# Optimization experiments

Measured on AMD Instinct MI355X. Metric: run time of the kernel, lower is better.

Reference implementation:

```python
import jax, jax.numpy as jnp
import numpy as np

V, E, H = 50000, 256, 256   # vocab, emb_dim, hid_dim
R, S, W = 64, 32, 64        # reviews, sentences/review, words/sentence
UF = 20                     # user feature dim


def _bigru_last(x, wih, whh, bih, bhh):
    """Bidirectional GRU over x [B,T,D]; returns sum of final hidden states of
    the two directions, shape [B,H]. Params stacked over direction axis 0."""
    Hh = whh.shape[-1]

    def onedir(xd, wi, wh, bi, bh):
        gx = jnp.einsum('btd,gd->btg', xd, wi) + bi  # [B,T,3H] input gates precomputed

        def step(h, gxt):
            gh = h @ wh.T + bh
            r = jax.nn.sigmoid(gxt[:, :Hh] + gh[:, :Hh])
            z = jax.nn.sigmoid(gxt[:, Hh:2 * Hh] + gh[:, Hh:2 * Hh])
            n = jnp.tanh(gxt[:, 2 * Hh:] + r * gh[:, 2 * Hh:])
            return (1.0 - z) * n + z * h, None

        h0 = jnp.zeros((xd.shape[0], Hh), xd.dtype)
        hT, _ = jax.lax.scan(step, h0, jnp.swapaxes(gx, 0, 1))
        return hT

    return (onedir(x, wih[0], whh[0], bih[0], bhh[0])
            + onedir(x[:, ::-1], wih[1], whh[1], bih[1], bhh[1]))


def setup_inputs() -> dict:
    key = jax.random.key(0)
    ks = iter(jax.random.split(key, 40))

    def wmat(shape, scale=0.05):
        return jax.random.normal(next(ks), shape, jnp.float32) * scale

    inp = {}
    inp['inputs'] = jax.random.randint(next(ks), (R, S, W), 0, V)
    inp['sent_lengths'] = jax.random.randint(next(ks), (R, S), 1, W)
    inp['sent_counts'] = jax.random.randint(next(ks), (R,), 1, S)
    inp['user_feats'] = jax.random.normal(next(ks), (R, UF), jnp.float32)
    inp['embed'] = wmat((V, E))
    for name, din in (('wg', E), ('sg', H), ('rg', H + UF)):
        inp[name + '_wih'] = wmat((2, 3 * H, din))
        inp[name + '_whh'] = wmat((2, 3 * H, H))
        inp[name + '_bih'] = jnp.zeros((2, 3 * H), jnp.float32)
        inp[name + '_bhh'] = jnp.zeros((2, 3 * H), jnp.float32)
    inp['rfc_w1'] = wmat((H // 2, H + UF)); inp['rfc_b1'] = jnp.zeros((H // 2,), jnp.float32)
    inp['rfc_w2'] = wmat((1, H // 2));      inp['rfc_b2'] = jnp.zeros((1,), jnp.float32)
    inp['pfc_w1'] = wmat((H // 2, H));      inp['pfc_b1'] = jnp.zeros((H // 2,), jnp.float32)
    inp['pfc_w2'] = wmat((9, H // 2));      inp['pfc_b2'] = jnp.zeros((9,), jnp.float32)
    inp['uf_w'] = jnp.ones((UF,), jnp.float32)  # user_feats_weights
    return inp


def reference(inputs, sent_lengths, sent_counts, user_feats, embed,
              wg_wih, wg_whh, wg_bih, wg_bhh,
              sg_wih, sg_whh, sg_bih, sg_bhh,
              rg_wih, rg_whh, rg_bih, rg_bhh,
              rfc_w1, rfc_b1, rfc_w2, rfc_b2,
              pfc_w1, pfc_b1, pfc_w2, pfc_b2, uf_w):
    Rr, Sr, Wr = inputs.shape
    emb = embed[inputs]  # [R,S,W,E]  (dropout = identity in eval mode)
    # word-level bi-GRU, all R*S sentences batched together
    sent = _bigru_last(emb.reshape(Rr * Sr, Wr, emb.shape[-1]),
                       wg_wih, wg_whh, wg_bih, wg_bhh).reshape(Rr, Sr, -1)
    # sentence-level bi-GRU, batch over reviews
    rev = _bigru_last(sent, sg_wih, sg_whh, sg_bih, sg_bhh)  # [R,H]
    # F.normalize(user_feats) * user_feats_weights
    nrm = jnp.maximum(jnp.linalg.norm(user_feats, axis=-1, keepdims=True), 1e-12)
    p_batch = jnp.concatenate([rev, (user_feats / nrm) * uf_w], axis=-1)  # [R,H+20]
    r_stars = (jax.nn.selu(p_batch @ rfc_w1.T + rfc_b1) @ rfc_w2.T + rfc_b2)[:, 0]  # [R]
    # review-level bi-GRU over the sequence of reviews (batch 1)
    doc = _bigru_last(p_batch[None], rg_wih, rg_whh, rg_bih, rg_bhh)[0]  # [H]
    p_stars = jax.nn.selu(doc @ pfc_w1.T + pfc_b1) @ pfc_w2.T + pfc_b2  # [9]
    return p_stars, r_stars
```

## Files before the change

kernel.cpp:

```cpp
#include <hip/hip_runtime.h>
#include <math.h>

#define R_ 64
#define S_ 32
#define W_ 64
#define H_ 256
#define UF_ 20
#define TC 4

typedef short bf16x8 __attribute__((ext_vector_type(8)));
typedef float f32x4  __attribute__((ext_vector_type(4)));

#define MFMA(a,b,c) __builtin_amdgcn_mfma_f32_16x16x32_bf16((a),(b),(c),0,0,0)

typedef const unsigned int __attribute__((address_space(1)))* gp_t;
typedef unsigned int __attribute__((address_space(3)))* lp_t;
#define GLOAD16(SRC, DST) \
  __builtin_amdgcn_global_load_lds((gp_t)(const void*)(SRC), (lp_t)(void*)(DST), 16, 0, 0)

#define SW(r) ((((r)>>1)&7)<<3)

#define BFRAG(ff) ((ff) < 40 ? Breg[(ff) < 40 ? (ff) : 0] \
                 : *(const bf16x8*)&Bl[w][(ff) >= 40 ? (ff)-40 : 0][l*8])

__device__ __forceinline__ float sigf(float x){ return 1.0f/(1.0f+__expf(-x)); }
__device__ __forceinline__ float tanhf_(float x){ float e=__expf(2.0f*x); return 1.0f-2.0f/(e+1.0f); }
__device__ __forceinline__ float seluf_(float x){
  const float sc=1.0507009873554805f, al=1.6732632423543772f;
  return x>0.0f ? sc*x : sc*al*(expf(x)-1.0f);
}
__device__ __forceinline__ short tobf(float f){
  unsigned u=__float_as_uint(f); u += 0x7fffu + ((u>>16)&1u); return (short)(u>>16);
}
__device__ __forceinline__ float bf2f(short s){
  return __uint_as_float(((unsigned)(unsigned short)s) << 16);
}
__device__ __forceinline__ unsigned pk2(float a, float b){
  return (unsigned)(unsigned short)tobf(a) | ((unsigned)(unsigned short)tobf(b) << 16);
}

__global__ void prep_word_w(const float* __restrict__ wih, const float* __restrict__ whh,
                            short* __restrict__ Bw)
{
  int idx = blockIdx.x*256 + threadIdx.x;
  int lane = idx & 63;
  int rest = idx >> 6;
  int f  = rest % 6;  rest /= 6;
  int kt = rest % 16; rest /= 16;
  int w  = rest % 8;
  int d  = rest / 8;
  int gate = f >> 1;
  int j = 32*w + (f&1)*16 + (lane&15);
  int row = gate*256 + j;
  const float* W = (kt < 8 ? wih : whh) + (size_t)d*768*256;
  int k = (kt&7)*32 + (lane>>4)*8;
  short* dst = Bw + ((((size_t)(d*8 + w)*16 + kt)*6 + f)*64 + lane)*8;
#pragma unroll
  for (int jj=0;jj<8;jj++) dst[jj] = tobf(W[(size_t)row*256 + k + jj]);
}

__global__ void prep_rnn_w(const float* __restrict__ whh, short* __restrict__ Bs)
{
  int idx = blockIdx.x*256 + threadIdx.x;
  int lane = idx & 63;
  int rest = idx >> 6;
  int f  = rest % 6; rest /= 6;
  int kt = rest % 8; rest /= 8;
  int w  = rest % 8;
  int d  = rest / 8;
  int j = 32*w + (f&1)*16 + (lane&15);
  int row = (f>>1)*256 + j;
  const float* W = whh + (size_t)d*768*256;
  int k = kt*32 + (lane>>4)*8;
  short* dst = Bs + ((((size_t)(d*8 + w)*8 + kt)*6 + f)*64 + lane)*8;
#pragma unroll
  for (int jj=0;jj<8;jj++) dst[jj] = tobf(W[(size_t)row*256 + k + jj]);
}

__global__ void prep_gemm_w(const float* __restrict__ Wsrc, short* __restrict__ Bg)
{
  int idx = blockIdx.x*256 + threadIdx.x;
  int lane = idx & 63;
  int rest = idx >> 6;
  int kt = rest % 8;
  int nt = rest / 8;
  int n = nt*16 + (lane&15);
  int k = kt*32 + (lane>>4)*8;
  short* dst = Bg + (((size_t)nt*8 + kt)*64 + lane)*8;
#pragma unroll
  for (int jj=0;jj<8;jj++) dst[jj] = tobf(Wsrc[(size_t)n*256 + k + jj]);
}

__global__ __launch_bounds__(256) void gemm_gxu(
    const short* __restrict__ Ab, const float* __restrict__ Af,
    const int* __restrict__ toks, const short* __restrict__ Bg,
    const float* __restrict__ bih, const float* __restrict__ bhh,
    short* __restrict__ C, long Czoff,
    int mode, int t0, int Mclamp, int Cstride)
{
  const int z  = blockIdx.z;
  const int m0 = blockIdx.x * 64;
  const int yt = blockIdx.y * 8;
  const int ntb = (mode == 2 ? z*48 : 0) + yt;
  const int tid = threadIdx.x;
  const int w = tid >> 6, l = tid & 63;
  const int c = l & 15, q = l >> 4;
  __shared__ short As[64][264];
  {
    const int row = tid >> 2, c0 = (tid & 3) * 64;
    if (mode == 0) {
      const uint4* s = (const uint4*)(Ab + (size_t)(m0+row)*256 + c0);
#pragma unroll
      for (int i = 0; i < 8; i++) *(uint4*)&As[row][c0 + i*8] = s[i];
    } else {
      int r;
      if (mode == 1) {
        r = m0 + row; if (r >= Mclamp) r = Mclamp - 1;
      } else {
        const int rr = m0 + row;
        const int s_ = rr / TC, i_ = rr % TC;
        const int wd = z ? (63 - (t0 + i_)) : (t0 + i_);
        r = toks[s_*64 + wd];
      }
      const float* s = Af + (size_t)r*256 + c0;
#pragma unroll
      for (int i = 0; i < 8; i++) {
        float4 v0 = *(const float4*)(s + i*8);
        float4 v1 = *(const float4*)(s + i*8 + 4);
        uint4 u;
        u.x = pk2(v0.x, v0.y); u.y = pk2(v0.z, v0.w);
        u.z = pk2(v1.x, v1.y); u.w = pk2(v1.z, v1.w);
        *(uint4*)&As[row][c0 + i*8] = u;
      }
    }
  }
  float bias[2];
#pragma unroll
  for (int nt = 0; nt < 2; nt++) {
    const int coln = (yt + 2*w + nt)*16 + c;
    const int bidx = (mode == 2 ? z*768 : 0) + coln;
    bias[nt] = bih[bidx] + ((bidx % 768) < 512 ? bhh[bidx] : 0.0f);
  }
  __syncthreads();
  f32x4 acc[4][2];
#pragma unroll
  for (int a = 0; a < 4; a++) { acc[a][0] = (f32x4)0.f; acc[a][1] = (f32x4)0.f; }
#pragma unroll
  for (int kt = 0; kt < 8; kt++) {
    const int ko = kt*32 + q*8;
    bf16x8 a0 = *(const bf16x8*)&As[ 0+c][ko];
    bf16x8 a1 = *(const bf16x8*)&As[16+c][ko];
    bf16x8 a2 = *(const bf16x8*)&As[32+c][ko];
    bf16x8 a3 = *(const bf16x8*)&As[48+c][ko];
    bf16x8 b0 = *(const bf16x8*)&Bg[(((size_t)(ntb + 2*w    )*8 + kt)*64 + l)*8];
    bf16x8 b1 = *(const bf16x8*)&Bg[(((size_t)(ntb + 2*w + 1)*8 + kt)*64 + l)*8];
    acc[0][0]=MFMA(a0,b0,acc[0][0]); acc[1][0]=MFMA(a1,b0,acc[1][0]);
    acc[2][0]=MFMA(a2,b0,acc[2][0]); acc[3][0]=MFMA(a3,b0,acc[3][0]);
    acc[0][1]=MFMA(a0,b1,acc[0][1]); acc[1][1]=MFMA(a1,b1,acc[1][1]);
    acc[2][1]=MFMA(a2,b1,acc[2][1]); acc[3][1]=MFMA(a3,b1,acc[3][1]);
  }
  short* Cz = C + (size_t)z * Czoff;
#pragma unroll
  for (int mt = 0; mt < 4; mt++)
#pragma unroll
  for (int nt = 0; nt < 2; nt++)
#pragma unroll
  for (int rg = 0; rg < 4; rg++)
    Cz[(size_t)(m0 + mt*16 + q*4 + rg)*Cstride + (yt + 2*w + nt)*16 + c] =
        tobf(acc[mt][nt][rg] + bias[nt]);
}

__device__ __forceinline__ void stage_issue(
    short* dstbase,
    int mode, int d, int g, int w, int l,
    int nwords, int t0, int tt,
    const int* tokp, const short* gxF, const short* gxB)
{
  const char* bF = (const char*)gxF;
  const char* bB = (const char*)gxB;
#pragma unroll
  for (int i = 0; i < 3; i++) {
    const int off = i*1024 + l*16;
    const int rl  = (off >= 1536) ? 1 : 0;
    const int col = off - rl*1536;
    const char* src;
    if (mode == 0) {
      const int tx  = d ? (nwords - 1 - tt) : tt;
      const int tok = tokp[(2*w + rl)*64 + tx];
      src = bF + (size_t)tok*3072 + d*1536 + col;
    } else if (mode == 1) {
      const int ri = (g*16 + 2*w + rl)*TC + (tt - t0);
      src = (d ? bB : bF) + (size_t)ri*1536 + col;
    } else {
      const int se  = d ? (nwords - 1 - tt) : tt;
      const int row = g*16 + 2*w + rl;
      src = bF + ((size_t)row*nwords + se)*3072 + (size_t)d*1536 + col;
    }
    GLOAD16(src, dstbase + (size_t)w*1536 + i*512);
  }
}

__global__ __launch_bounds__(512, 2) void gru_rec(
    const int* __restrict__ toks,
    const short* __restrict__ gxF, const short* __restrict__ gxB,
    const short* __restrict__ Bh, int wstride, int koff,
    const float* __restrict__ bhh,
    float* __restrict__ hstate, int NS,
    int t0, int nsteps, int mode, int nwords)
{
  const int d = blockIdx.x & 1;
  const int g = blockIdx.x >> 1;
  const int tid = threadIdx.x;
  const int w = tid >> 6, l = tid & 63;
  const int c = l & 15, q = l >> 4;

  __shared__ short gbuf[2][16][768];
  __shared__ short hbf[2][16][264];
  __shared__ short Bl[8][8][512];
  __shared__ int   tokL[1024];

  if (mode == 0)
    for (int i = tid; i < 1024; i += 512) tokL[i] = toks[(size_t)g*1024 + i];

  bf16x8 Breg[40];
  {
    const short* Bb = Bh + (size_t)(d*8 + w)*wstride + (size_t)koff*3072 + l*8;
#pragma unroll
    for (int ff = 0; ff < 48; ff++) {
      bf16x8 v = *(const bf16x8*)(Bb + ff*512);
      if (ff < 40) Breg[ff] = v;
      else *(bf16x8*)&Bl[w][ff-40][l*8] = v;
    }
  }

  float bNH[2];
#pragma unroll
  for (int jt = 0; jt < 2; jt++)
    bNH[jt] = bhh[d*768 + 512 + 32*w + jt*16 + c];

  float hst[2][4];
  const int cur0 = t0 & 1;
  if (t0 == 0) {
#pragma unroll
    for (int a = 0; a < 2; a++)
#pragma unroll
    for (int r = 0; r < 4; r++) hst[a][r] = 0.0f;
  } else {
#pragma unroll
    for (int jt = 0; jt < 2; jt++)
#pragma unroll
    for (int rg = 0; rg < 4; rg++)
      hst[jt][rg] = hstate[((size_t)d*NS + g*16 + q*4 + rg)*256 + 32*w + jt*16 + c];
  }
#pragma unroll
  for (int jt = 0; jt < 2; jt++)
#pragma unroll
  for (int rg = 0; rg < 4; rg++)
    hbf[cur0][q*4 + rg][32*w + jt*16 + c] = tobf(hst[jt][rg]);

  stage_issue((short*)gbuf[cur0], mode, d, g, w, l, nwords, t0, t0,
              (mode == 0) ? toks + (size_t)g*1024 : (const int*)nullptr, gxF, gxB);

  __syncthreads();

  const int tend = t0 + nsteps;
  for (int t = t0; t < tend; t++) {
    const int cur = t & 1, nxt = 1 - cur;

    if (t + 1 < tend)
      stage_issue((short*)gbuf[nxt], mode, d, g, w, l, nwords, t0, t + 1,
                  tokL, gxF, gxB);

    f32x4 accR[2], accZ[2], accNH[2];
#pragma unroll
    for (int a = 0; a < 2; a++) { accR[a]=(f32x4)0.f; accZ[a]=(f32x4)0.f; accNH[a]=(f32x4)0.f; }
#pragma unroll
    for (int kt = 0; kt < 8; kt++) {
      bf16x8 a0 = *(const bf16x8*)&hbf[cur][c][kt*32 + q*8];
      bf16x8 b0 = BFRAG(kt*6+0), b1 = BFRAG(kt*6+1), b2 = BFRAG(kt*6+2),
             b3 = BFRAG(kt*6+3), b4 = BFRAG(kt*6+4), b5 = BFRAG(kt*6+5);
      accR[0]=MFMA(a0,b0,accR[0]);  accR[1]=MFMA(a0,b1,accR[1]);
      accZ[0]=MFMA(a0,b2,accZ[0]);  accZ[1]=MFMA(a0,b3,accZ[1]);
      accNH[0]=MFMA(a0,b4,accNH[0]); accNH[1]=MFMA(a0,b5,accNH[1]);
    }

#pragma unroll
    for (int jt = 0; jt < 2; jt++)
#pragma unroll
    for (int rg = 0; rg < 4; rg++) {
      const int m = q*4 + rg;
      const int j = 32*w + jt*16 + c;
      const float gr = bf2f(gbuf[cur][m][j]);
      const float gz = bf2f(gbuf[cur][m][256 + j]);
      const float gn = bf2f(gbuf[cur][m][512 + j]);
      const float r = sigf(gr + accR[jt][rg]);
      const float z = sigf(gz + accZ[jt][rg]);
      const float n = tanhf_(gn + r*(accNH[jt][rg] + bNH[jt]));
      float h = hst[jt][rg];
      h = (1.0f - z)*n + z*h;
      hst[jt][rg] = h;
      hbf[nxt][m][j] = tobf(h);
    }
    __syncthreads();
  }

#pragma unroll
  for (int jt = 0; jt < 2; jt++)
#pragma unroll
  for (int rg = 0; rg < 4; rg++)
    hstate[((size_t)d*NS + g*16 + q*4 + rg)*256 + 32*w + jt*16 + c] = hst[jt][rg];
}

__global__ void add2bf(const float* __restrict__ a, const float* __restrict__ b,
                       short* __restrict__ o)
{
  int i = (blockIdx.x*256 + threadIdx.x)*4;
  float4 x = *(const float4*)&a[i];
  float4 y = *(const float4*)&b[i];
  *(uint2*)&o[i] = make_uint2(pk2(x.x+y.x, x.y+y.y), pk2(x.z+y.z, x.w+y.w));
}

__global__ __launch_bounds__(512, 2) void rev_gru(
    const float* __restrict__ gx, const short* __restrict__ Br,
    const float* __restrict__ bhh,
    float* __restrict__ doc)
{
  const int d = blockIdx.x;
  const int tid = threadIdx.x;
  const int w = tid >> 6, l = tid & 63;
  const int c = l & 15, q = l >> 4;
  const int j0 = 32*w + c;

  __shared__ short hbf[2][16][256];
  __shared__ short Bl[8][8][512];
  for (int i = tid; i < 2*16*256; i += 512) ((short*)hbf)[i] = 0;

  bf16x8 Breg[40];
  {
    const short* Bbase = Br + (size_t)(d*8 + w)*8*6*512 + l*8;
#pragma unroll
    for (int ff = 0; ff < 48; ff++) {
      bf16x8 v = *(const bf16x8*)(Bbase + ff*512);
      if (ff < 40) Breg[ff] = v;
      else *(bf16x8*)&Bl[w][ff-40][l*8] = v;
    }
  }

  float bNH[2];
#pragma unroll
  for (int jt = 0; jt < 2; jt++)
    bNH[jt] = bhh[d*768 + 512 + j0 + jt*16];

  float hst[2];
  hst[0] = 0.0f; hst[1] = 0.0f;
  __syncthreads();

  for (int t = 0; t < 64; t++) {
    const int cur = t & 1, nxt = 1 - cur;
    const int teff = (d == 0) ? t : (63 - t);

    float G[2][3];
    if (q == 0) {
#pragma unroll
      for (int jt = 0; jt < 2; jt++) {
        const size_t row = (size_t)teff*1536 + d*768;
        const int j = j0 + jt*16;
        G[jt][0] = gx[row + j]; G[jt][1] = gx[row + 256 + j]; G[jt][2] = gx[row + 512 + j];
      }
    }

    f32x4 accR[2], accZ[2], accNH[2];
#pragma unroll
    for (int a=0;a<2;a++) { accR[a]=(f32x4)0.f; accZ[a]=(f32x4)0.f; accNH[a]=(f32x4)0.f; }
#pragma unroll
    for (int kt = 0; kt < 8; kt++) {
      bf16x8 a0 = *(const bf16x8*)&hbf[cur][c][(kt*32 + q*8) ^ SW(c)];
      bf16x8 b0 = BFRAG(kt*6+0), b1 = BFRAG(kt*6+1), b2 = BFRAG(kt*6+2),
             b3 = BFRAG(kt*6+3), b4 = BFRAG(kt*6+4), b5 = BFRAG(kt*6+5);
      accR[0]=MFMA(a0,b0,accR[0]);  accR[1]=MFMA(a0,b1,accR[1]);
      accZ[0]=MFMA(a0,b2,accZ[0]);  accZ[1]=MFMA(a0,b3,accZ[1]);
      accNH[0]=MFMA(a0,b4,accNH[0]); accNH[1]=MFMA(a0,b5,accNH[1]);
    }

    if (q == 0) {
#pragma unroll
      for (int jt = 0; jt < 2; jt++) {
        const float r = sigf(G[jt][0] + accR[jt][0]);
        const float z = sigf(G[jt][1] + accZ[jt][0]);
        const float n = tanhf_(G[jt][2] + r*(accNH[jt][0] + bNH[jt]));
        const float h = n + z*(hst[jt] - n);
        hst[jt] = h;
        hbf[nxt][0][j0 + jt*16] = tobf(h);
      }
    }
    __syncthreads();
  }
  if (q == 0) {
#pragma unroll
    for (int jt = 0; jt < 2; jt++)
      doc[d*256 + j0 + jt*16] = hst[jt];
  }
}

__global__ __launch_bounds__(256) void gemm_nt16(
    const float* __restrict__ A, const float* __restrict__ B,
    const float* __restrict__ bih, const float* __restrict__ bhh,
    float* __restrict__ C, int M, int N, int K)
{
  const int m0 = blockIdx.x * 16;
  const int n0 = blockIdx.y * 64;
  const int tid = threadIdx.x;
  __shared__ float As[16][17];
  __shared__ float Bs[16][68];
  float acc[4] = {0,0,0,0};
  const int m  = tid >> 4, n4 = (tid & 15) * 4;
  const int bn = tid >> 2, bk = (tid & 3) * 4;
  for (int k0 = 0; k0 < K; k0 += 16) {
    const int ak = tid & 15;
    float av = (k0 + ak < K) ? A[(size_t)(m0+m)*K + k0 + ak] : 0.0f;
    float4 b4 = make_float4(0,0,0,0);
    if (k0 + bk < K) b4 = *(const float4*)&B[(size_t)(n0+bn)*K + k0 + bk];
    __syncthreads();
    As[ak][m] = av;
    Bs[bk+0][bn]=b4.x; Bs[bk+1][bn]=b4.y; Bs[bk+2][bn]=b4.z; Bs[bk+3][bn]=b4.w;
    __syncthreads();
#pragma unroll
    for (int k = 0; k < 16; k++) {
      const float a = As[k][m];
      const float4 bb = *(const float4*)&Bs[k][n4];
      acc[0]+=a*bb.x; acc[1]+=a*bb.y; acc[2]+=a*bb.z; acc[3]+=a*bb.w;
    }
  }
#pragma unroll
  for (int i = 0; i < 4; i++) {
    const int n = n0 + n4 + i;
    acc[i] += bih[n] + ((n % 768) < 512 ? bhh[n] : 0.0f);
  }
  *(float4*)&C[(size_t)(m0+m)*N + n0+n4] = make_float4(acc[0],acc[1],acc[2],acc[3]);
}

__global__ void pbatch_k(const float* __restrict__ hs, const float* __restrict__ uf,
                         const float* __restrict__ ufw, float* __restrict__ pb)
{
  const int r = blockIdx.x, tid = threadIdx.x;
  __shared__ float nrm;
  if (tid == 0) {
    float s = 0.f;
    for (int i = 0; i < UF_; i++) { const float v = uf[r*UF_ + i]; s += v*v; }
    nrm = fmaxf(sqrtf(s), 1e-12f);
  }
  __syncthreads();
  if (tid < H_)  pb[r*276 + tid] = hs[r*H_ + tid] + hs[(size_t)R_*H_ + r*H_ + tid];
  if (tid < UF_) pb[r*276 + H_ + tid] = uf[r*UF_ + tid] / nrm * ufw[tid];
}

__global__ void rstars_k(const float* __restrict__ pb,
                         const float* __restrict__ w1, const float* __restrict__ b1,
                         const float* __restrict__ w2, const float* __restrict__ b2,
                         float* __restrict__ out)
{
  const int r = blockIdx.x, tid = threadIdx.x;
  __shared__ float ps[276];
  __shared__ float s1[128];
  for (int i = tid; i < 276; i += 128) ps[i] = pb[r*276 + i];
  __syncthreads();
  float a = b1[tid];
  for (int k = 0; k < 276; k++) a += ps[k] * w1[tid*276 + k];
  s1[tid] = seluf_(a);
  __syncthreads();
  if (tid == 0) {
    float s = b2[0];
    for (int k = 0; k < 128; k++) s += s1[k] * w2[k];
    out[9 + r] = s;
  }
}

__global__ void pstars_k(const float* __restrict__ doc2,
                         const float* __restrict__ w1, const float* __restrict__ b1,
                         const float* __restrict__ w2, const float* __restrict__ b2,
                         float* __restrict__ out)
{
  const int tid = threadIdx.x;
  __shared__ float dc[256];
  __shared__ float s1[128];
  dc[tid]       = doc2[tid];
  dc[128 + tid] = doc2[128 + tid];
  __syncthreads();
  float a = b1[tid];
  for (int k = 0; k < 256; k++) a += dc[k] * w1[tid*256 + k];
  s1[tid] = seluf_(a);
  __syncthreads();
  if (tid < 9) {
    float s = b2[tid];
    for (int k = 0; k < 128; k++) s += s1[k] * w2[tid*128 + k];
    out[tid] = s;
  }
}

__global__ void docsum_k(float* __restrict__ doc)
{
  const int tid = threadIdx.x;
  doc[tid] = doc[tid] + doc[256 + tid];
}

extern "C" void kernel_launch(void* const* d_in, const int* in_sizes, int n_in,
                              void* d_out, int out_size, void* d_ws, size_t ws_size,
                              hipStream_t stream)
{
  const int*   toks   = (const int*)  d_in[0];
  const float* uf     = (const float*)d_in[3];
  const float* embed  = (const float*)d_in[4];
  const float* wg_wih = (const float*)d_in[5];
  const float* wg_whh = (const float*)d_in[6];
  const float* wg_bih = (const float*)d_in[7];
  const float* wg_bhh = (const float*)d_in[8];
  const float* sg_wih = (const float*)d_in[9];
  const float* sg_whh = (const float*)d_in[10];
  const float* sg_bih = (const float*)d_in[11];
  const float* sg_bhh = (const float*)d_in[12];
  const float* rg_wih = (const float*)d_in[13];
  const float* rg_whh = (const float*)d_in[14];
  const float* rg_bih = (const float*)d_in[15];
  const float* rg_bhh = (const float*)d_in[16];
  const float* rfc_w1 = (const float*)d_in[17];
  const float* rfc_b1 = (const float*)d_in[18];
  const float* rfc_w2 = (const float*)d_in[19];
  const float* rfc_b2 = (const float*)d_in[20];
  const float* pfc_w1 = (const float*)d_in[21];
  const float* pfc_b1 = (const float*)d_in[22];
  const float* pfc_w2 = (const float*)d_in[23];
  const float* pfc_b2 = (const float*)d_in[24];
  const float* uf_w   = (const float*)d_in[25];
  float* out = (float*)d_out;
  float* ws  = (float*)d_ws;
  (void)in_sizes; (void)n_in; (void)out_size;

  const size_t OFF_BW   = 0;
  const size_t OFF_BS   = OFF_BW  + 393216;
  const size_t OFF_BR   = OFF_BS  + 196608;
  const size_t OFF_BG   = OFF_BR  + 196608;
  const size_t OFF_BGW  = OFF_BG  + 196608;
  const size_t OFF_HF   = OFF_BGW + 196608;
  const size_t OFF_SB   = OFF_HF  + 1048576;
  const size_t OFF_GXS  = OFF_SB  + 262144;
  const size_t OFF_HS   = OFF_GXS + 1572864;
  const size_t OFF_PB   = OFF_HS  + 32768;
  const size_t OFF_GXR  = OFF_PB  + 17664;
  const size_t OFF_DOC  = OFF_GXR + 98304;
  const size_t OFF_GXT  = OFF_DOC + 512;
  const size_t TOT_A    = OFF_GXT + (size_t)50048*1536/2;

  short* Bw   = (short*)(ws + OFF_BW);
  short* Bs   = (short*)(ws + OFF_BS);
  short* Br   = (short*)(ws + OFF_BR);
  short* Bg   = (short*)(ws + OFF_BG);
  short* Bgw  = (short*)(ws + OFF_BGW);
  float* hfin = ws + OFF_HF;
  short* sentb= (short*)(ws + OFF_SB);
  short* gxs  = (short*)(ws + OFF_GXS);
  float* hs   = ws + OFF_HS;
  float* pb   = ws + OFF_PB;
  float* gxr  = ws + OFF_GXR;
  float* doc  = ws + OFF_DOC;
  short* gxf  = (short*)(ws + OFF_GXT);
  short* gxb  = gxf + (size_t)8192*768;
  short* gxv  = (short*)(ws + OFF_GXT);

  const bool big = ws_size >= TOT_A * sizeof(float);

  prep_word_w<<<384, 256, 0, stream>>>(wg_wih, wg_whh, Bw);
  prep_rnn_w<<<192, 256, 0, stream>>>(sg_whh, Bs);
  prep_rnn_w<<<192, 256, 0, stream>>>(rg_whh, Br);
  prep_gemm_w<<<192, 256, 0, stream>>>(sg_wih, Bg);
  prep_gemm_w<<<192, 256, 0, stream>>>(wg_wih, Bgw);

  if (big) {
    gemm_gxu<<<dim3(782, 12, 1), 256, 0, stream>>>(
        nullptr, embed, nullptr, Bgw, wg_bih, wg_bhh, gxv, 0, 1, 0, 50000, 1536);
    gru_rec<<<256, 512, 0, stream>>>(toks, gxv, nullptr, Bw, 49152, 8,
        wg_bhh, hfin, 2048, 0, 64, 0, 64);
  } else {
    for (int tc = 0; tc < 64/TC; tc++) {
      gemm_gxu<<<dim3(128, 6, 2), 256, 0, stream>>>(
          nullptr, embed, toks, Bgw, wg_bih, wg_bhh, gxf, (long)8192*768, 2, tc*TC, 0, 768);
      gru_rec<<<256, 512, 0, stream>>>(toks, gxf, gxb, Bw, 49152, 8,
          wg_bhh, hfin, 2048, tc*TC, TC, 1, 64);
    }
  }
  add2bf<<<512, 256, 0, stream>>>(hfin, hfin + (size_t)2048*256, sentb);

  gemm_gxu<<<dim3(32, 12, 1), 256, 0, stream>>>(
      sentb, nullptr, nullptr, Bg, sg_bih, sg_bhh, gxs, 0, 0, 0, 2048, 1536);
  gru_rec<<<8, 512, 0, stream>>>(nullptr, gxs, nullptr, Bs, 24576, 0,
      sg_bhh, hs, 64, 0, 32, 2, 32);

  pbatch_k<<<R_, 256, 0, stream>>>(hs, uf, uf_w, pb);
  rstars_k<<<R_, 128, 0, stream>>>(pb, rfc_w1, rfc_b1, rfc_w2, rfc_b2, out);

  gemm_nt16<<<dim3(4, 24), 256, 0, stream>>>(pb, rg_wih, rg_bih, rg_bhh, gxr, 64, 1536, 276);
  rev_gru<<<2, 512, 0, stream>>>(gxr, Br, rg_bhh, doc);
  docsum_k<<<1, 256, 0, stream>>>(doc);
  pstars_k<<<1, 128, 0, stream>>>(doc, pfc_w1, pfc_b1, pfc_w2, pfc_b2, out);
}
```

Before: 706.3 us.

## Add dedicated vocab-table GEMM kernel and fuse small epilogue kernels

Replaces the generic gemm_gxu launch that precomputes input gates for the entire 50000-row vocabulary with a new gemm_gxv kernel. Each 512-thread block converts a 128-row slab of embeddings to bf16 once in LDS, then loops over all 1536 output columns in six passes, so A is not reloaded per column tile. It also fuses pbatch with the review-stars MLP and folds the doc direction sum into pstars, which removes two launches. In exchange the new kernel uses large LDS and register tiles, which lowers occupancy, and it writes C with scattered bf16 stores.

```diff
diff --git a/kernel.cpp b/kernel.cpp
--- a/kernel.cpp
+++ b/kernel.cpp
@@ -89,6 +89,66 @@
   short* dst = Bg + (((size_t)nt*8 + kt)*64 + lane)*8;
 #pragma unroll
   for (int jj=0;jj<8;jj++) dst[jj] = tobf(Wsrc[(size_t)n*256 + k + jj]);
+}
+
+__global__ __launch_bounds__(512) void gemm_gxv(
+    const float* __restrict__ Af, const short* __restrict__ Bg,
+    const float* __restrict__ bih, const float* __restrict__ bhh,
+    short* __restrict__ C, int Mclamp)
+{
+  const int m0 = blockIdx.x * 128;
+  const int tid = threadIdx.x;
+  const int w = tid >> 6, l = tid & 63;
+  const int c = l & 15, q = l >> 4;
+  __shared__ short As[128][264];
+  {
+    const int row = tid >> 2, c0 = (tid & 3) * 64;
+    int r = m0 + row; if (r >= Mclamp) r = Mclamp - 1;
+    const float* s = Af + (size_t)r*256 + c0;
+#pragma unroll
+    for (int i = 0; i < 8; i++) {
+      float4 v0 = *(const float4*)(s + i*8);
+      float4 v1 = *(const float4*)(s + i*8 + 4);
+      uint4 u;
+      u.x = pk2(v0.x, v0.y); u.y = pk2(v0.z, v0.w);
+      u.z = pk2(v1.x, v1.y); u.w = pk2(v1.z, v1.w);
+      *(uint4*)&As[row][c0 + i*8] = u;
+    }
+  }
+  __syncthreads();
+
+  for (int pass = 0; pass < 6; pass++) {
+    const int ntb = pass*16 + w*2;
+    float bias[2];
+#pragma unroll
+    for (int nt = 0; nt < 2; nt++) {
+      const int bidx = (ntb + nt)*16 + c;
+      bias[nt] = bih[bidx] + ((bidx % 768) < 512 ? bhh[bidx] : 0.0f);
+    }
+    f32x4 acc[8][2];
+#pragma unroll
+    for (int mt = 0; mt < 8; mt++) { acc[mt][0] = (f32x4)0.f; acc[mt][1] = (f32x4)0.f; }
+#pragma unroll
+    for (int kt = 0; kt < 8; kt++) {
+      const int ko = kt*32 + q*8;
+      bf16x8 b0 = *(const bf16x8*)&Bg[(((size_t)(ntb    )*8 + kt)*64 + l)*8];
+      bf16x8 b1 = *(const bf16x8*)&Bg[(((size_t)(ntb + 1)*8 + kt)*64 + l)*8];
+#pragma unroll
+      for (int mt = 0; mt < 8; mt++) {
+        bf16x8 a = *(const bf16x8*)&As[mt*16 + c][ko];
+        acc[mt][0] = MFMA(a, b0, acc[mt][0]);
+        acc[mt][1] = MFMA(a, b1, acc[mt][1]);
+      }
+    }
+#pragma unroll
+    for (int mt = 0; mt < 8; mt++)
+#pragma unroll
+    for (int nt = 0; nt < 2; nt++)
+#pragma unroll
+    for (int rg = 0; rg < 4; rg++)
+      C[(size_t)(m0 + mt*16 + q*4 + rg)*1536 + (ntb + nt)*16 + c] =
+          tobf(acc[mt][nt][rg] + bias[nt]);
+  }
 }
 
 __global__ __launch_bounds__(256) void gemm_gxu(
@@ -439,10 +499,15 @@
   *(float4*)&C[(size_t)(m0+m)*N + n0+n4] = make_float4(acc[0],acc[1],acc[2],acc[3]);
 }
 
-__global__ void pbatch_k(const float* __restrict__ hs, const float* __restrict__ uf,
-                         const float* __restrict__ ufw, float* __restrict__ pb)
+__global__ void pbrs_k(const float* __restrict__ hs, const float* __restrict__ uf,
+                       const float* __restrict__ ufw,
+                       const float* __restrict__ w1, const float* __restrict__ b1,
+                       const float* __restrict__ w2, const float* __restrict__ b2,
+                       float* __restrict__ pb, float* __restrict__ out)
 {
   const int r = blockIdx.x, tid = threadIdx.x;
+  __shared__ float ps[276];
+  __shared__ float s1[128];
   __shared__ float nrm;
   if (tid == 0) {
     float s = 0.f;
@@ -450,23 +515,20 @@
     nrm = fmaxf(sqrtf(s), 1e-12f);
   }
   __syncthreads();
-  if (tid < H_)  pb[r*276 + tid] = hs[r*H_ + tid] + hs[(size_t)R_*H_ + r*H_ + tid];
-  if (tid < UF_) pb[r*276 + H_ + tid] = uf[r*UF_ + tid] / nrm * ufw[tid];
-}
-
-__global__ void rstars_k(const float* __restrict__ pb,
-                         const float* __restrict__ w1, const float* __restrict__ b1,
-                         const float* __restrict__ w2, const float* __restrict__ b2,
-                         float* __restrict__ out)
-{
-  const int r = blockIdx.x, tid = threadIdx.x;
-  __shared__ float ps[276];
-  __shared__ float s1[128];
-  for (int i = tid; i < 276; i += 128) ps[i] = pb[r*276 + i];
-  __syncthreads();
-  float a = b1[tid];
-  for (int k = 0; k < 276; k++) a += ps[k] * w1[tid*276 + k];
-  s1[tid] = seluf_(a);
+  if (tid < H_) {
+    const float v = hs[r*H_ + tid] + hs[(size_t)R_*H_ + r*H_ + tid];
+    ps[tid] = v; pb[r*276 + tid] = v;
+  }
+  if (tid < UF_) {
+    const float v = uf[r*UF_ + tid] / nrm * ufw[tid];
+    ps[H_ + tid] = v; pb[r*276 + H_ + tid] = v;
+  }
+  __syncthreads();
+  if (tid < 128) {
+    float a = b1[tid];
+    for (int k = 0; k < 276; k++) a += ps[k] * w1[tid*276 + k];
+    s1[tid] = seluf_(a);
+  }
   __syncthreads();
   if (tid == 0) {
     float s = b2[0];
@@ -483,8 +545,8 @@
   const int tid = threadIdx.x;
   __shared__ float dc[256];
   __shared__ float s1[128];
-  dc[tid]       = doc2[tid];
-  dc[128 + tid] = doc2[128 + tid];
+  dc[tid]       = doc2[tid]       + doc2[256 + tid];
+  dc[128 + tid] = doc2[128 + tid] + doc2[384 + tid];
   __syncthreads();
   float a = b1[tid];
   for (int k = 0; k < 256; k++) a += dc[k] * w1[tid*256 + k];
@@ -495,12 +557,6 @@
     for (int k = 0; k < 128; k++) s += s1[k] * w2[tid*128 + k];
     out[tid] = s;
   }
-}
-
-__global__ void docsum_k(float* __restrict__ doc)
-{
-  const int tid = threadIdx.x;
-  doc[tid] = doc[tid] + doc[256 + tid];
 }
 
 extern "C" void kernel_launch(void* const* d_in, const int* in_sizes, int n_in,
@@ -575,8 +631,7 @@
   prep_gemm_w<<<192, 256, 0, stream>>>(wg_wih, Bgw);
 
   if (big) {
-    gemm_gxu<<<dim3(782, 12, 1), 256, 0, stream>>>(
-        nullptr, embed, nullptr, Bgw, wg_bih, wg_bhh, gxv, 0, 1, 0, 50000, 1536);
+    gemm_gxv<<<391, 512, 0, stream>>>(embed, Bgw, wg_bih, wg_bhh, gxv, 50000);
     gru_rec<<<256, 512, 0, stream>>>(toks, gxv, nullptr, Bw, 49152, 8,
         wg_bhh, hfin, 2048, 0, 64, 0, 64);
   } else {
@@ -594,11 +649,9 @@
   gru_rec<<<8, 512, 0, stream>>>(nullptr, gxs, nullptr, Bs, 24576, 0,
       sg_bhh, hs, 64, 0, 32, 2, 32);
 
-  pbatch_k<<<R_, 256, 0, stream>>>(hs, uf, uf_w, pb);
-  rstars_k<<<R_, 128, 0, stream>>>(pb, rfc_w1, rfc_b1, rfc_w2, rfc_b2, out);
+  pbrs_k<<<R_, 256, 0, stream>>>(hs, uf, uf_w, rfc_w1, rfc_b1, rfc_w2, rfc_b2, pb, out);
 
   gemm_nt16<<<dim3(4, 24), 256, 0, stream>>>(pb, rg_wih, rg_bih, rg_bhh, gxr, 64, 1536, 276);
   rev_gru<<<2, 512, 0, stream>>>(gxr, Br, rg_bhh, doc);
-  docsum_k<<<1, 256, 0, stream>>>(doc);
   pstars_k<<<1, 128, 0, stream>>>(doc, pfc_w1, pfc_b1, pfc_w2, pfc_b2, out);
 }
```

Result: slower. 805.3 us (+14.0%).
